# Optimization experiments

Hardware: AMD Instinct MI355X
Metric: run time of the kernel (lower is better)

Reference implementation:

```python
import jax, jax.numpy as jnp
import numpy as np

NEG_SLOPE = 0.1  # negative slope of LeakyReLU in Conv3dReLU/Conv2dReLU


def setup_inputs() -> dict:
    key = jax.random.key(0)
    ks = jax.random.split(key, 16)
    B, C, PREV, N, M1, M2 = 2, 16, 16, 16384, 4096, 4096
    D1, CORR, FILT = 4, 15, 15          # d1 = d+1; (r+1)^d1 - r^d1 with r=1
    CO0, CO1 = 32, 32                    # num_corr_output
    O0, O1 = 64, 64                      # num_output
    CIN = 2 * C + PREV                   # corr_conv input channels

    feat1 = jax.random.normal(ks[0], (B, C, M1), jnp.float32)
    feat2 = jax.random.normal(ks[1], (B, C, M2), jnp.float32)
    prev_corr_feat = jax.random.normal(ks[2], (B, PREV, N), jnp.float32)
    barycentric1 = jax.random.uniform(ks[3], (B, D1, N), jnp.float32)
    # lattice_offset1: batch-offset flattened indices into [0, B*(M1+1)); value -1+1=0 is the pad slot
    local = jax.random.randint(ks[4], (B, D1, N), 0, M1)
    lattice_offset1 = local + (jnp.arange(B, dtype=jnp.int64) * (M1 + 1))[:, None, None]
    pc1_corr_indices = jax.random.randint(ks[5], (B, CORR, M1), -1, M1).astype(jnp.int64)
    pc2_corr_indices = jax.random.randint(ks[6], (B, FILT, CORR, M1), -1, M2).astype(jnp.int64)

    s = 0.05
    cw0 = jax.random.normal(ks[7], (CO0, CIN, CORR), jnp.float32) * s   # Conv3d (1,corr_size,1)
    cb0 = jax.random.normal(ks[8], (CO0,), jnp.float32) * s
    cw1 = jax.random.normal(ks[9], (CO1, CO0), jnp.float32) * s        # Conv3d 1x1x1
    cb1 = jax.random.normal(ks[10], (CO1,), jnp.float32) * s
    bw0 = jax.random.normal(ks[11], (O0, CO1, FILT), jnp.float32) * s  # Conv2d (filter_size,1)
    bb0 = jax.random.normal(ks[12], (O0,), jnp.float32) * s
    bw1 = jax.random.normal(ks[13], (O1, O0), jnp.float32) * s         # Conv2d 1x1 (no relu)
    bb1 = jax.random.normal(ks[14], (O1,), jnp.float32) * s

    return {
        "feat1": feat1, "feat2": feat2, "prev_corr_feat": prev_corr_feat,
        "barycentric1": barycentric1,
        "cw0": cw0, "cb0": cb0, "cw1": cw1, "cb1": cb1,
        "bw0": bw0, "bb0": bb0, "bw1": bw1, "bb1": bb1,
        "lattice_offset1": lattice_offset1,
        "pc1_corr_indices": pc1_corr_indices,
        "pc2_corr_indices": pc2_corr_indices,
        "max_hash_cnt1": M1, "max_hash_cnt2": M2,
    }


def reference(feat1, feat2, prev_corr_feat, barycentric1,
              cw0, cb0, cw1, cb1, bw0, bb0, bw1, bb1,
              lattice_offset1, pc1_corr_indices, pc2_corr_indices,
              max_hash_cnt1, max_hash_cnt2):
    B, C, M1 = feat1.shape
    PREV = prev_corr_feat.shape[1]

    # ---- splat prev_corr_feat onto lattice vertices (scatter-add) ----
    flat_idx = (lattice_offset1 + 1).reshape(-1)                      # (B*d1*N,)
    # (B, PREV, d1, N) -> (B, d1, N, PREV) -> (B*d1*N, PREV)
    vals = (barycentric1[:, None, :, :] * prev_corr_feat[:, :, None, :])
    vals = vals.transpose(0, 2, 3, 1).reshape(-1, PREV)
    prev_splat = jax.ops.segment_sum(vals, flat_idx, num_segments=B * (M1 + 1))
    prev_splat = prev_splat.reshape(B, M1 + 1, PREV).transpose(0, 2, 1)  # (B, PREV, M1+1)

    # use_norm: normalize by splatted barycentric mass
    ones_splat = jax.ops.segment_sum(barycentric1.reshape(-1), flat_idx,
                                     num_segments=B * (M1 + 1)).reshape(B, M1 + 1)
    prev_splat = prev_splat * (1.0 / (ones_splat + 1e-5))[:, None, :]

    # ---- prepend zero pad slot (index 0 catches -1 neighbor indices) ----
    splat1 = jnp.concatenate([prev_splat, jnp.pad(feat1, ((0, 0), (0, 0), (1, 0)))], axis=1)  # (B, PREV+C, M1+1)
    splat2 = jnp.pad(feat2, ((0, 0), (0, 0), (1, 0)))                                          # (B, C, M2+1)

    # ---- irregular gathers ----
    g1 = jax.vmap(lambda s, i: s[:, i])(splat1, pc1_corr_indices + 1)   # (B, PREV+C, corr, M1)
    g2 = jax.vmap(lambda s, i: s[:, i])(splat2, pc2_corr_indices + 1)   # (B, C, filt, corr, M1)
    FILT = g2.shape[2]
    g1b = jnp.broadcast_to(g1[:, :, None], (B, g1.shape[1], FILT, g1.shape[2], M1))
    combined = jnp.concatenate([g1b, g2], axis=1)                       # (B, 2C+PREV, filt, corr, M1)

    # ---- corr_conv: Conv3d(1,corr,1)+LeakyReLU, then 1x1x1+LeakyReLU ----
    x = jnp.einsum('bifkn,oik->bofn', combined, cw0) + cb0[None, :, None, None]
    x = jax.nn.leaky_relu(x, NEG_SLOPE)
    x = jnp.einsum('bcfn,oc->bofn', x, cw1) + cb1[None, :, None, None]
    x = jax.nn.leaky_relu(x, NEG_SLOPE)

    # ---- blur_conv: Conv2d(filt,1)+LeakyReLU, then 1x1 (last_relu=False) ----
    y = jnp.einsum('bcfn,ocf->bon', x, bw0) + bb0[None, :, None]
    y = jax.nn.leaky_relu(y, NEG_SLOPE)
    y = jnp.einsum('bcn,oc->bon', y, bw1) + bb1[None, :, None]
    return y
```

## Files before the change

### kernel.cpp

```cpp
#include <hip/hip_runtime.h>
#include <hip/hip_bf16.h>

namespace {

constexpr int B     = 2;
constexpr int C     = 16;
constexpr int PREVC = 16;
constexpr int NPTS  = 16384;
constexpr int M1    = 4096;
constexpr int D1    = 4;
constexpr int CORR  = 15;
constexpr int FILT  = 15;
constexpr int CIN   = 48;
constexpr int CO0   = 32;
constexpr int O1    = 64;
constexpr int MS    = M1 + 1;
constexpr int NSLOT = B * MS;
constexpr int NPAIR = B * D1 * NPTS;
constexpr int BCAP  = 64;
constexpr int GSTR  = 240;
constexpr float NEG = 0.1f;

constexpr size_t OFF_SP1   = 0;
constexpr size_t SZ_SP1    = (size_t)NSLOT * 32;
constexpr size_t OFF_SP2   = OFF_SP1 + SZ_SP1;
constexpr size_t SZ_SP2    = (size_t)NSLOT * 16;
constexpr size_t OFF_P     = OFF_SP2 + SZ_SP2;
constexpr size_t SZ_PQ     = (size_t)B * CORR * MS * 32 / 2;
constexpr size_t OFF_Q     = OFF_P + SZ_PQ;
constexpr size_t OFF_CWT   = OFF_Q + SZ_PQ;
constexpr size_t SZ_CWT    = (size_t)CORR * CIN * 32;
constexpr size_t OFF_W0R   = OFF_CWT + SZ_CWT;
constexpr size_t SZ_W0R    = 512 * 64;
constexpr size_t OFF_PREVT = OFF_W0R + SZ_W0R;
constexpr size_t SZ_PREVT  = (size_t)B * NPTS * 16;
constexpr size_t OFF_CNT   = OFF_PREVT + SZ_PREVT;
constexpr size_t SZ_CNT    = 8208;
constexpr size_t OFF_REC   = OFF_CNT + SZ_CNT;
constexpr size_t SZ_REC    = (size_t)NSLOT * BCAP;
constexpr size_t OFF_GT    = OFF_REC + SZ_REC;
constexpr size_t SZ_GT     = (size_t)B * M1 * GSTR;

__device__ __forceinline__ float leaky(float v) { return v > 0.f ? v : NEG * v; }
__device__ __forceinline__ float bflo(unsigned u) { return __uint_as_float(u << 16); }
__device__ __forceinline__ float bfhi(unsigned u) { return __uint_as_float(u & 0xffff0000u); }

__global__ __launch_bounds__(256) void k_pre(const int* __restrict__ lo,
                                             const float* __restrict__ prev,
                                             const float* __restrict__ cw0,
                                             const float* __restrict__ bw0,
                                             const int* __restrict__ pc1,
                                             const int* __restrict__ pc2,
                                             int* __restrict__ counts,
                                             int* __restrict__ rec,
                                             float* __restrict__ prevT,
                                             float* __restrict__ cwT,
                                             float* __restrict__ W0r,
                                             unsigned int* __restrict__ gT) {
  int bx = blockIdx.x, tid = threadIdx.x;
  if (bx < 512) {
    int t = bx * 256 + tid;
    int slot = lo[t] + 1;
    int pos = atomicAdd(counts + slot, 1);
    if (pos < BCAP) rec[slot * BCAP + pos] = t;
  } else if (bx < 1024) {
    __shared__ float tile[16][65];
    int bb = bx - 512;
    int b = bb >> 8, n0 = (bb & 255) * 64;
    for (int e = tid; e < 1024; e += 256) {
      int ln = e & 63, r = e >> 6;
      tile[r][ln] = prev[((size_t)b * PREVC + r) * NPTS + n0 + ln];
    }
    __syncthreads();
    for (int e = tid; e < 1024; e += 256) {
      int c = e & 15, nn = e >> 4;
      prevT[((size_t)b * NPTS + n0 + nn) * 16 + c] = tile[c][nn];
    }
  } else if (bx < 1243) {
    int e = (bx - 1024) * 256 + tid;
    if (e < CORR * CIN * 32) {
      int o = e & 31, i = (e >> 5) % CIN, k = e / (CIN * 32);
      cwT[e] = cw0[((size_t)o * CIN + i) * CORR + k];
    }
    int e2 = e - CORR * CIN * 32;
    if (e2 >= 0 && e2 < 512 * 64) {
      int o3 = e2 & 63, cf = e2 >> 6, c = cf >> 4, f = cf & 15;
      W0r[e2] = (f < FILT) ? bw0[((size_t)o3 * CO0 + c) * FILT + f] : 0.f;
    }
  } else {
    __shared__ int tile[16][65];
    int t = bx - 1243;
    int n0 = (t & 63) * 64;
    int rest = t >> 6;
    int b = rest & 1;
    int rt = rest >> 1;
    const int* src; int r0, nr, doff;
    if (rt < 15) { src = pc2 + (size_t)b * FILT * CORR * M1; r0 = rt * 16;
                   nr = min(16, FILT * CORR - r0); doff = 0; }
    else         { src = pc1 + (size_t)b * CORR * M1; r0 = 0; nr = CORR; doff = 225; }
    for (int e = tid; e < nr * 64; e += 256) {
      int ln = e & 63, r = e >> 6;
      tile[r][ln] = src[(size_t)(r0 + r) * M1 + n0 + ln] + 1;
    }
    __syncthreads();
    for (int e = tid; e < 1024; e += 256) {
      int rr = e & 15, nn = e >> 4;
      if (rr < nr)
        gT[((size_t)b * M1 + n0 + nn) * GSTR + doff + r0 + rr] =
            (unsigned int)(tile[rr][nn] * 64);
    }
  }
}

__global__ __launch_bounds__(256) void k_sum(const int* __restrict__ rec,
                                             const int* __restrict__ counts,
                                             const float* __restrict__ bary,
                                             const float* __restrict__ prevT,
                                             const float* __restrict__ feat1,
                                             const float* __restrict__ feat2,
                                             float* __restrict__ splat1,
                                             float* __restrict__ splat2) {
  int tid = threadIdx.x;
  int s = blockIdx.x * 4 + (tid >> 6);
  if (s >= NSLOT) return;
  int lane = tid & 63, c = lane & 15, g = lane >> 4;
  int cnt = min(counts[s], BCAP);
  const int* bucket = rec + (size_t)s * BCAP;
  float acc = 0.f, wsum = 0.f;
  for (int e = g; e < cnt; e += 4) {
    int t = bucket[e];
    float w = bary[t];
    int n = t & (NPTS - 1);
    int b = t >> 16;
    acc += w * prevT[((size_t)b * NPTS + n) * 16 + c];
    wsum += w;
  }
  acc  += __shfl_down(acc, 32);  acc  += __shfl_down(acc, 16);
  wsum += __shfl_down(wsum, 32); wsum += __shfl_down(wsum, 16);
  if (lane < 16) {
    int m = s % MS, b2 = s / MS;
    float scale = 1.f / (wsum + 1e-5f);
    splat1[(size_t)s * 32 + c] = acc * scale;
    float f1 = (m == 0) ? 0.f : feat1[((size_t)b2 * C + c) * M1 + (m - 1)];
    splat1[(size_t)s * 32 + 16 + c] = f1;
    float f2 = (m == 0) ? 0.f : feat2[((size_t)b2 * C + c) * M1 + (m - 1)];
    splat2[(size_t)s * 16 + c] = f2;
  }
}

__global__ __launch_bounds__(256) void k_pq(const float* __restrict__ sp1,
                                            const float* __restrict__ sp2,
                                            const float* __restrict__ cwT,
                                            __hip_bfloat16* __restrict__ Pt,
                                            __hip_bfloat16* __restrict__ Qt) {
  __shared__ float wk[CIN][33];
  int k = blockIdx.y, b = blockIdx.z;
  int tid = threadIdx.x;
  int m0 = blockIdx.x * 64;
  int mm = tid >> 4, o2 = tid & 15;
  for (int e = tid; e < CIN * 32; e += 256)
    wk[e >> 5][e & 31] = cwT[(size_t)k * CIN * 32 + e];
  __syncthreads();
  int oa = o2 * 2, ob = oa + 1;
#pragma unroll
  for (int mt = 0; mt < 4; ++mt) {
    int m = m0 + mt * 16 + mm;
    if (m >= MS) continue;
    const float* s1 = sp1 + ((size_t)b * MS + m) * 32;
    const float* s2 = sp2 + ((size_t)b * MS + m) * 16;
    float q0 = 0, q1 = 0, p0 = 0, p1 = 0;
#pragma unroll
    for (int i4 = 0; i4 < 8; ++i4) {
      float4 s = *(const float4*)(s1 + i4 * 4);
      q0 += s.x * wk[i4*4+0][oa] + s.y * wk[i4*4+1][oa] + s.z * wk[i4*4+2][oa] + s.w * wk[i4*4+3][oa];
      q1 += s.x * wk[i4*4+0][ob] + s.y * wk[i4*4+1][ob] + s.z * wk[i4*4+2][ob] + s.w * wk[i4*4+3][ob];
    }
#pragma unroll
    for (int i4 = 0; i4 < 4; ++i4) {
      float4 s = *(const float4*)(s2 + i4 * 4);
      p0 += s.x * wk[32+i4*4+0][oa] + s.y * wk[32+i4*4+1][oa] + s.z * wk[32+i4*4+2][oa] + s.w * wk[32+i4*4+3][oa];
      p1 += s.x * wk[32+i4*4+0][ob] + s.y * wk[32+i4*4+1][ob] + s.z * wk[32+i4*4+2][ob] + s.w * wk[32+i4*4+3][ob];
    }
    size_t base = ((size_t)(b * CORR + k) * MS + m) * 32;
    __hip_bfloat162 qq, pp;
    qq.x = __float2bfloat16(q0); qq.y = __float2bfloat16(q1);
    pp.x = __float2bfloat16(p0); pp.y = __float2bfloat16(p1);
    *reinterpret_cast<__hip_bfloat162*>(Qt + base + oa) = qq;
    *reinterpret_cast<__hip_bfloat162*>(Pt + base + oa) = pp;
  }
}

__global__ __launch_bounds__(256, 4) void k_gather(const __hip_bfloat16* __restrict__ Pt,
                                                   const __hip_bfloat16* __restrict__ Qt,
                                                   const unsigned int* __restrict__ gT,
                                                   const float* __restrict__ cw1,
                                                   const float* __restrict__ cb0,
                                                   const float* __restrict__ cb1,
                                                   const float* __restrict__ W0r,
                                                   const float* __restrict__ bb0,
                                                   const float* __restrict__ bw1,
                                                   const float* __restrict__ bb1,
                                                   float* __restrict__ out) {
  __shared__ __attribute__((aligned(16))) char smem[19072];
  unsigned int* idxs = (unsigned int*)smem;
  float* parts       = (float*)smem;
  float* p1s         = (float*)(smem + 4096);
  float* xls         = (float*)(smem + 4608);
  float* wch         = (float*)(smem + 4608);
  __hip_bfloat16* hT = (__hip_bfloat16*)(smem + 13824);
  float* y0s         = (float*)(smem + 17984);

  int bid = blockIdx.x;
  int b = (bid >> 2) & 1;
  int r = bid & 3, x = bid >> 3;
  int n0 = (r << 10) | (x << 2);
  int pt0 = (b << 12) | n0;
  int tid = threadIdx.x;

  for (int e = tid; e < 240; e += 256) {
    int pl = e / 60, d = e - pl * 60;
    ((uint4*)(idxs + pl * GSTR))[d] =
        ((const uint4*)(gT + (size_t)(pt0 + pl) * GSTR))[d];
  }
  __syncthreads();

  int pl = tid >> 6, lane = tid & 63;

  {
    int f = lane >> 2, o4 = lane & 3;
    const char* base = (const char*)((f < CORR ? Pt : Qt) + (size_t)b * CORR * MS * 32);
    const unsigned int* ip = idxs + pl * GSTR + (f < CORR ? f * CORR : 225);
    unsigned int lo = (unsigned int)(o4 * 16);
    float a[8] = {};
#pragma unroll
    for (int k = 0; k < CORR; ++k) {
      unsigned int off = ip[k] + (unsigned int)(k * MS * 64) + lo;
      uint4 d = *(const uint4*)(base + off);
      a[0] += bflo(d.x); a[1] += bfhi(d.x);
      a[2] += bflo(d.y); a[3] += bfhi(d.y);
      a[4] += bflo(d.z); a[5] += bfhi(d.z);
      a[6] += bflo(d.w); a[7] += bfhi(d.w);
    }
    if (f == CORR) {
#pragma unroll
      for (int j = 0; j < 8; ++j)
        p1s[pl * 32 + o4 * 8 + j] = a[j] + cb0[o4 * 8 + j];
    }
    __syncthreads();
    if (f < CORR) {
#pragma unroll
      for (int j = 0; j < 8; ++j)
        xls[pl * 576 + f * 36 + o4 * 8 + j] = leaky(a[j] + p1s[pl * 32 + o4 * 8 + j]);
    }
  }
  __syncthreads();

  {
    int o = lane & 31, fh = lane >> 5;
    const float* wrow = cw1 + o * CO0;
    float bias = cb1[o];
    float h[8];
#pragma unroll
    for (int j = 0; j < 8; ++j) {
      float hh = bias;
#pragma unroll
      for (int c4 = 0; c4 < 8; ++c4) {
        float4 xv = *(const float4*)&xls[pl * 576 + (fh * 8 + j) * 36 + c4 * 4];
        float4 w  = *(const float4*)(wrow + c4 * 4);
        hh += w.x * xv.x + w.y * xv.y + w.z * xv.z + w.w * xv.w;
      }
      h[j] = leaky(hh);
    }
    if (fh == 1) h[7] = 0.f;
    union { __hip_bfloat16 hb[8]; uint4 u; } pk;
#pragma unroll
    for (int j = 0; j < 8; ++j) pk.hb[j] = __float2bfloat16(h[j]);
    *(uint4*)(hT + pl * 520 + o * 16 + fh * 8) = pk.u;
  }

  int og = tid & 15, bpl = (tid >> 4) & 3, rep = tid >> 6;
  float acc[4] = {};
  for (int kc = 0; kc < 512; kc += 32) {
    __syncthreads();
    for (int e = tid; e < 512; e += 256) {
      int rr = e >> 4, c4 = e & 15;
      *(float4*)&wch[rr * 68 + c4 * 4] = *(const float4*)(W0r + (size_t)(kc + rr) * 64 + c4 * 4);
    }
    __syncthreads();
#pragma unroll
    for (int i = 0; i < 8; ++i) {
      int kk = rep + i * 4;
      float hv = __bfloat162float(hT[bpl * 520 + kc + kk]);
      float4 w = *(const float4*)&wch[kk * 68 + og * 4];
      acc[0] += w.x * hv; acc[1] += w.y * hv; acc[2] += w.z * hv; acc[3] += w.w * hv;
    }
  }
  __syncthreads();
  *(float4*)&parts[((rep * 4 + bpl) * 16 + og) * 4] = make_float4(acc[0], acc[1], acc[2], acc[3]);
  __syncthreads();

  {
    int ypl = tid & 3, yo3 = tid >> 2;
    int og2 = yo3 >> 2, comp = yo3 & 3;
    float y0 = bb0[yo3];
#pragma unroll
    for (int rp = 0; rp < 4; ++rp)
      y0 += parts[((rp * 4 + ypl) * 16 + og2) * 4 + comp];
    y0s[ypl * 68 + yo3] = leaky(y0);
  }
  __syncthreads();

  {
    int fpl = tid & 3, fo1 = tid >> 2;
    const float* w1row = bw1 + fo1 * 64;
    float y1 = bb1[fo1];
#pragma unroll
    for (int c4 = 0; c4 < 16; ++c4) {
      float4 w = *(const float4*)(w1row + c4 * 4);
      y1 += w.x * y0s[fpl * 68 + c4 * 4 + 0] + w.y * y0s[fpl * 68 + c4 * 4 + 1] +
            w.z * y0s[fpl * 68 + c4 * 4 + 2] + w.w * y0s[fpl * 68 + c4 * 4 + 3];
    }
    out[((size_t)(b * O1 + fo1)) * M1 + n0 + fpl] = y1;
  }
}

}

extern "C" void kernel_launch(void* const* d_in, const int* in_sizes, int n_in,
                              void* d_out, int out_size, void* d_ws, size_t ws_size,
                              hipStream_t stream) {
  const float* feat1 = (const float*)d_in[0];
  const float* feat2 = (const float*)d_in[1];
  const float* prev  = (const float*)d_in[2];
  const float* bary  = (const float*)d_in[3];
  const float* cw0   = (const float*)d_in[4];
  const float* cb0   = (const float*)d_in[5];
  const float* cw1   = (const float*)d_in[6];
  const float* cb1   = (const float*)d_in[7];
  const float* bw0   = (const float*)d_in[8];
  const float* bb0   = (const float*)d_in[9];
  const float* bw1   = (const float*)d_in[10];
  const float* bb1   = (const float*)d_in[11];
  const int* lo  = (const int*)d_in[12];
  const int* pc1 = (const int*)d_in[13];
  const int* pc2 = (const int*)d_in[14];

  float* ws = (float*)d_ws;
  float* splat1 = ws + OFF_SP1;
  float* splat2 = ws + OFF_SP2;
  __hip_bfloat16* Pt = (__hip_bfloat16*)(ws + OFF_P);
  __hip_bfloat16* Qt = (__hip_bfloat16*)(ws + OFF_Q);
  float* cwT   = ws + OFF_CWT;
  float* W0r   = ws + OFF_W0R;
  float* prevT = ws + OFF_PREVT;
  int* counts  = (int*)(ws + OFF_CNT);
  int* rec     = (int*)(ws + OFF_REC);
  unsigned int* gT = (unsigned int*)(ws + OFF_GT);
  float* out   = (float*)d_out;

  hipMemsetAsync(counts, 0, NSLOT * sizeof(int), stream);

  hipLaunchKernelGGL(k_pre, dim3(1243 + 2048), dim3(256), 0, stream,
                     lo, prev, cw0, bw0, pc1, pc2, counts, rec, prevT, cwT, W0r, gT);
  hipLaunchKernelGGL(k_sum, dim3((NSLOT + 3) / 4), dim3(256), 0, stream,
                     rec, counts, bary, prevT, feat1, feat2, splat1, splat2);
  hipLaunchKernelGGL(k_pq, dim3((MS + 63) / 64, CORR, B), dim3(256), 0, stream,
                     splat1, splat2, cwT, Pt, Qt);
  hipLaunchKernelGGL(k_gather, dim3(B * M1 / 4), dim3(256), 0, stream,
                     Pt, Qt, gT, cw1, cb0, cb1, W0r, bb0, bw1, bb1, out);
}
```

Before: 111.9 us.

## Stage correlation gathers into LDS with direct global-to-LDS loads

The 15 per-lane bf16 gathers from the P/Q tables in k_gather now use global_load_lds and land directly in a per-wave 15 KB LDS slab. A single vmcnt wait follows, and the values are then read back from LDS for the reduction. Shared memory grows to 64 KB and is re-laid out into per-wave slabs, and the launch bound drops from 4 to 2 blocks per CU. The aim is to keep all gathers in flight without holding them in VGPRs, at the cost of lower occupancy and an extra LDS round trip.

```diff
diff --git a/kernel.cpp b/kernel.cpp
--- a/kernel.cpp
+++ b/kernel.cpp
@@ -19,6 +19,7 @@
 constexpr int NPAIR = B * D1 * NPTS;
 constexpr int BCAP  = 64;
 constexpr int GSTR  = 240;
+constexpr int SLAB  = 15360;
 constexpr float NEG = 0.1f;
 
 constexpr size_t OFF_SP1   = 0;
@@ -44,6 +45,12 @@
 __device__ __forceinline__ float leaky(float v) { return v > 0.f ? v : NEG * v; }
 __device__ __forceinline__ float bflo(unsigned u) { return __uint_as_float(u << 16); }
 __device__ __forceinline__ float bfhi(unsigned u) { return __uint_as_float(u & 0xffff0000u); }
+
+__device__ __forceinline__ void gload_lds16(const void* g, void* l) {
+  __builtin_amdgcn_global_load_lds(
+      (const __attribute__((address_space(1))) unsigned int*)g,
+      (__attribute__((address_space(3))) unsigned int*)l, 16, 0, 0);
+}
 
 __global__ __launch_bounds__(256) void k_pre(const int* __restrict__ lo,
                                              const float* __restrict__ prev,
@@ -190,7 +197,7 @@
   }
 }
 
-__global__ __launch_bounds__(256, 4) void k_gather(const __hip_bfloat16* __restrict__ Pt,
+__global__ __launch_bounds__(256, 2) void k_gather(const __hip_bfloat16* __restrict__ Pt,
                                                    const __hip_bfloat16* __restrict__ Qt,
                                                    const unsigned int* __restrict__ gT,
                                                    const float* __restrict__ cw1,
@@ -201,14 +208,11 @@
                                                    const float* __restrict__ bw1,
                                                    const float* __restrict__ bb1,
                                                    float* __restrict__ out) {
-  __shared__ __attribute__((aligned(16))) char smem[19072];
-  unsigned int* idxs = (unsigned int*)smem;
-  float* parts       = (float*)smem;
-  float* p1s         = (float*)(smem + 4096);
-  float* xls         = (float*)(smem + 4608);
-  float* wch         = (float*)(smem + 4608);
-  __hip_bfloat16* hT = (__hip_bfloat16*)(smem + 13824);
-  float* y0s         = (float*)(smem + 17984);
+  __shared__ __attribute__((aligned(16))) char smem[65536];
+  unsigned int* idxs = (unsigned int*)(smem + 61440);
+  float* parts       = (float*)(smem + 61440);
+  float* wch         = (float*)(smem + 6144);
+  float* y0s         = (float*)(smem + SLAB + 6144);
 
   int bid = blockIdx.x;
   int b = (bid >> 2) & 1;
@@ -225,17 +229,28 @@
   __syncthreads();
 
   int pl = tid >> 6, lane = tid & 63;
+  char* slabp = smem + pl * SLAB;
+  float* xlsP = (float*)slabp;
+  __hip_bfloat16* hTp = (__hip_bfloat16*)(slabp + 4096 + pl * 80);
+  float* p1sP = (float*)(slabp + 5632);
 
   {
     int f = lane >> 2, o4 = lane & 3;
-    const char* base = (const char*)((f < CORR ? Pt : Qt) + (size_t)b * CORR * MS * 32);
+    const char* baseg = (const char*)((f < CORR ? Pt : Qt) + (size_t)b * CORR * MS * 32);
     const unsigned int* ip = idxs + pl * GSTR + (f < CORR ? f * CORR : 225);
     unsigned int lo = (unsigned int)(o4 * 16);
-    float a[8] = {};
 #pragma unroll
     for (int k = 0; k < CORR; ++k) {
       unsigned int off = ip[k] + (unsigned int)(k * MS * 64) + lo;
-      uint4 d = *(const uint4*)(base + off);
+      gload_lds16(baseg + off, slabp + k * 1024);
+    }
+    asm volatile("s_waitcnt vmcnt(0)" ::: "memory");
+    __builtin_amdgcn_sched_barrier(0);
+
+    float a[8] = {};
+#pragma unroll
+    for (int k = 0; k < CORR; ++k) {
+      uint4 d = *(const uint4*)(slabp + k * 1024 + lane * 16);
       a[0] += bflo(d.x); a[1] += bfhi(d.x);
       a[2] += bflo(d.y); a[3] += bfhi(d.y);
       a[4] += bflo(d.z); a[5] += bfhi(d.z);
@@ -244,13 +259,13 @@
     if (f == CORR) {
 #pragma unroll
       for (int j = 0; j < 8; ++j)
-        p1s[pl * 32 + o4 * 8 + j] = a[j] + cb0[o4 * 8 + j];
+        p1sP[o4 * 8 + j] = a[j] + cb0[o4 * 8 + j];
     }
     __syncthreads();
     if (f < CORR) {
 #pragma unroll
       for (int j = 0; j < 8; ++j)
-        xls[pl * 576 + f * 36 + o4 * 8 + j] = leaky(a[j] + p1s[pl * 32 + o4 * 8 + j]);
+        xlsP[f * 36 + o4 * 8 + j] = leaky(a[j] + p1sP[o4 * 8 + j]);
     }
   }
   __syncthreads();
@@ -265,7 +280,7 @@
       float hh = bias;
 #pragma unroll
       for (int c4 = 0; c4 < 8; ++c4) {
-        float4 xv = *(const float4*)&xls[pl * 576 + (fh * 8 + j) * 36 + c4 * 4];
+        float4 xv = *(const float4*)&xlsP[(fh * 8 + j) * 36 + c4 * 4];
         float4 w  = *(const float4*)(wrow + c4 * 4);
         hh += w.x * xv.x + w.y * xv.y + w.z * xv.z + w.w * xv.w;
       }
@@ -275,10 +290,11 @@
     union { __hip_bfloat16 hb[8]; uint4 u; } pk;
 #pragma unroll
     for (int j = 0; j < 8; ++j) pk.hb[j] = __float2bfloat16(h[j]);
-    *(uint4*)(hT + pl * 520 + o * 16 + fh * 8) = pk.u;
+    *(uint4*)(hTp + o * 16 + fh * 8) = pk.u;
   }
 
   int og = tid & 15, bpl = (tid >> 4) & 3, rep = tid >> 6;
+  const __hip_bfloat16* hTb = (const __hip_bfloat16*)(smem + bpl * SLAB + 4096 + bpl * 80);
   float acc[4] = {};
   for (int kc = 0; kc < 512; kc += 32) {
     __syncthreads();
@@ -290,7 +306,7 @@
 #pragma unroll
     for (int i = 0; i < 8; ++i) {
       int kk = rep + i * 4;
-      float hv = __bfloat162float(hT[bpl * 520 + kc + kk]);
+      float hv = __bfloat162float(hTb[kc + kk]);
       float4 w = *(const float4*)&wch[kk * 68 + og * 4];
       acc[0] += w.x * hv; acc[1] += w.y * hv; acc[2] += w.z * hv; acc[3] += w.w * hv;
     }
```

Result: slower. 143.1 us (+27.9%).
